# Kernel tuning notes

Hardware: AMD Instinct MI355X
Metric: run time of the kernel (lower is better)

The kernel has to match this reference:

```python
import jax, jax.numpy as jnp
import numpy as np

KERNEL_MUL = 2.0
KERNEL_NUM = 5


def setup_inputs() -> dict:
    key = jax.random.key(0)
    k1, k2 = jax.random.split(key)
    source = jax.random.normal(k1, (4096, 256), dtype=jnp.float32)
    target = jax.random.normal(k2, (4096, 256), dtype=jnp.float32)
    return {"source": source, "target": target}


def reference(source, target):
    n = source.shape[0]
    total = jnp.concatenate([source, target], axis=0)  # [2N, D]
    ns = total.shape[0]
    # Squared-L2 pairwise distances via the GEMM trick (avoids [2N,2N,D] blowup)
    sq = jnp.sum(total * total, axis=1)  # [2N]
    dist = sq[:, None] + sq[None, :] - 2.0 * (total @ total.T)  # [2N,2N]
    # bandwidth computed on detached distances (torch uses .data)
    bandwidth = jax.lax.stop_gradient(jnp.sum(dist)) / (ns * ns - ns)
    bandwidth = bandwidth / (KERNEL_MUL ** (KERNEL_NUM // 2))
    # multi-bandwidth Gaussian kernel sum (small fixed loop over KERNEL_NUM)
    kernels = jnp.zeros_like(dist)
    for i in range(KERNEL_NUM):
        kernels = kernels + jnp.exp(-dist / (bandwidth * (KERNEL_MUL ** i)))
    kernels = kernels / KERNEL_NUM
    XX = kernels[:n, :n]
    YY = kernels[n:, n:]
    XY = kernels[:n, n:]
    YX = kernels[n:, :n]
    # symmetric == 'yes' branch
    return jnp.mean(XX + YY - XY - YX) / 2.0
```

## Files before the change

### kernel.cpp

```cpp
#include <hip/hip_runtime.h>

#define NROWS 8192
#define NHALF 4096
#define DIM   256
#define NB_PREP 256
#define NTILES  64
#define NBLK    2080

typedef __attribute__((ext_vector_type(4))) float f32x4;

__device__ __forceinline__ const float* side_base(const float* src, const float* tgt, int row) {
    return (row < NHALF) ? (src + (size_t)row * DIM)
                         : (tgt + (size_t)(row - NHALF) * DIM);
}

__global__ __launch_bounds__(256) void prep_kernel(
        const float* __restrict__ src, const float* __restrict__ tgt,
        unsigned char* __restrict__ F8,
        float* __restrict__ sq, float* __restrict__ colpart, float* __restrict__ sqpart)
{
    int t = threadIdx.x;
    int lane = t & 63;
    int w = t >> 6;
    int wave = blockIdx.x * 4 + w;
    float cs0 = 0, cs1 = 0, cs2 = 0, cs3 = 0;
    double lss = 0.0;
    for (int r = wave; r < NROWS; r += NB_PREP * 4) {
        const float* p = side_base(src, tgt, r);
        float4 v = *(const float4*)(p + 4 * lane);
        cs0 += v.x; cs1 += v.y; cs2 += v.z; cs3 += v.w;
        int p01 = __builtin_amdgcn_cvt_pk_fp8_f32(v.x, v.y, 0, false);
        int pk  = __builtin_amdgcn_cvt_pk_fp8_f32(v.z, v.w, p01, true);
        *(unsigned*)(F8 + (size_t)r * DIM + 4 * lane) = (unsigned)pk;
        float d = v.x * v.x + v.y * v.y + v.z * v.z + v.w * v.w;
        #pragma unroll
        for (int off = 32; off > 0; off >>= 1) d += __shfl_xor(d, off);
        if (lane == 0) { sq[r] = d; lss += (double)d; }
    }
    __shared__ float csh[4][256];
    __shared__ double ssh[4];
    csh[w][4 * lane + 0] = cs0; csh[w][4 * lane + 1] = cs1;
    csh[w][4 * lane + 2] = cs2; csh[w][4 * lane + 3] = cs3;
    if (lane == 0) ssh[w] = lss;
    __syncthreads();
    colpart[blockIdx.x * 256 + t] = csh[0][t] + csh[1][t] + csh[2][t] + csh[3][t];
    if (t == 0) sqpart[blockIdx.x] = (float)(ssh[0] + ssh[1] + ssh[2] + ssh[3]);
}

__global__ void bw_kernel(const float* __restrict__ colpart,
                          const float* __restrict__ sqpart, float* __restrict__ qconst)
{
    __shared__ double red[256], red2[256];
    int t = threadIdx.x;
    double s = 0;
    for (int b = 0; b < NB_PREP; ++b) s += (double)colpart[b * 256 + t];
    red[t] = s * s;
    red2[t] = (double)sqpart[t];
    __syncthreads();
    for (int k = 128; k > 0; k >>= 1) {
        if (t < k) { red[t] += red[t + k]; red2[t] += red2[t + k]; }
        __syncthreads();
    }
    if (t == 0) {
        double ns = (double)NROWS;
        double sumdist = 2.0 * ns * red2[0] - 2.0 * red[0];
        double bw = sumdist / (ns * ns - ns) / 4.0;
        qconst[0] = (float)(1.4426950408889634 / (16.0 * bw));
    }
}

__device__ __forceinline__ int tri_cum(int b) {
    return b * NTILES - ((b * (b - 1)) >> 1);
}

__global__ __launch_bounds__(256) void mmd_main_kernel(
        const unsigned char* __restrict__ F8,
        const float* __restrict__ sq, const float* __restrict__ qc,
        float* __restrict__ partials)
{
    __shared__ alignas(16) char lds[65536];

    int wg = blockIdx.x;
    int rank = (wg & 7) * (NBLK / 8) + (wg >> 3);
    int by = (int)((129.0f - sqrtf(16641.0f - 8.0f * (float)rank)) * 0.5f);
    while (tri_cum(by + 1) <= rank) ++by;
    while (tri_cum(by) > rank) --by;
    int bx = by + (rank - tri_cum(by));

    int t = threadIdx.x;
    int rowBase = by * 128, colBase = bx * 128;
    int lane = t & 63, w = t >> 6;
    int wr = w >> 1, wc = w & 1;

    #pragma unroll
    for (int q = 0; q < 8; ++q) {
        int p = q * 4096 + t * 16;
        int row = p >> 8;
        int col = (p & 255) ^ ((row & 7) << 4);
        const char* ga = (const char*)F8 + (((size_t)(rowBase + row)) << 8) + col;
        const char* gb = (const char*)F8 + (((size_t)(colBase + row)) << 8) + col;
        __builtin_amdgcn_global_load_lds(
            (const __attribute__((address_space(1))) void*)ga,
            (__attribute__((address_space(3))) void*)(lds + p), 16, 0, 0);
        __builtin_amdgcn_global_load_lds(
            (const __attribute__((address_space(1))) void*)gb,
            (__attribute__((address_space(3))) void*)(lds + 32768 + p), 16, 0, 0);
    }
    __syncthreads();

    f32x4 acc[4][4];
    #pragma unroll
    for (int m = 0; m < 4; ++m)
        #pragma unroll
        for (int n = 0; n < 4; ++n) acc[m][n] = (f32x4)0.f;

    #pragma unroll
    for (int kk = 0; kk < 8; ++kk) {
        int kcol = kk * 32 + ((lane >> 4) << 3);
        long long af[4], bf[4];
        #pragma unroll
        for (int m = 0; m < 4; ++m) {
            int r = wr * 64 + m * 16 + (lane & 15);
            int off = ((r << 8) + kcol) ^ ((r & 7) << 4);
            af[m] = *(const long long*)(lds + off);
        }
        #pragma unroll
        for (int n = 0; n < 4; ++n) {
            int r = wc * 64 + n * 16 + (lane & 15);
            int off = ((r << 8) + kcol) ^ ((r & 7) << 4);
            bf[n] = *(const long long*)(lds + 32768 + off);
        }
        #pragma unroll
        for (int m = 0; m < 4; ++m)
            #pragma unroll
            for (int n = 0; n < 4; ++n)
                acc[m][n] = __builtin_amdgcn_mfma_f32_16x16x32_fp8_fp8(
                    af[m], bf[n], acc[m][n], 0, 0, 0);
    }

    float q = qc[0], twoq = 2.f * q;
    int rsub = (lane >> 4) * 4, csub = lane & 15;
    float nqa[4][4], qb[4];
    #pragma unroll
    for (int m = 0; m < 4; ++m)
        #pragma unroll
        for (int r = 0; r < 4; ++r)
            nqa[m][r] = -q * sq[rowBase + wr * 64 + m * 16 + rsub + r];
    #pragma unroll
    for (int n = 0; n < 4; ++n)
        qb[n] = q * sq[colBase + wc * 64 + n * 16 + csub];

    float psum = 0.f;
    #pragma unroll
    for (int m = 0; m < 4; ++m) {
        #pragma unroll
        for (int n = 0; n < 4; ++n) {
            #pragma unroll
            for (int r = 0; r < 4; ++r) {
                float arg = fmaf(acc[m][n][r], twoq, nqa[m][r] - qb[n]);
                float e4 = __builtin_amdgcn_exp2f(arg);
                float e3 = e4 * e4, e2 = e3 * e3, e1 = e2 * e2, e0 = e1 * e1;
                psum += ((e4 + e3) + (e2 + e1)) + e0;
            }
        }
    }

    #pragma unroll
    for (int off = 32; off > 0; off >>= 1) psum += __shfl_xor(psum, off);
    __syncthreads();
    float* redw = (float*)lds;
    if (lane == 0) redw[w] = psum;
    __syncthreads();
    if (t == 0) {
        float sign = ((rowBase < NHALF) == (colBase < NHALF)) ? 1.f : -1.f;
        float wgt = (bx == by) ? 1.f : 2.f;
        partials[rank] = sign * wgt * (redw[0] + redw[1] + redw[2] + redw[3]);
    }
}

__global__ void finalize_kernel(const float* __restrict__ partials, int n,
                                float* __restrict__ out)
{
    __shared__ double red[256];
    int t = threadIdx.x;
    double s = 0;
    for (int i = t; i < n; i += 256) s += (double)partials[i];
    red[t] = s;
    __syncthreads();
    for (int k = 128; k > 0; k >>= 1) { if (t < k) red[t] += red[t + k]; __syncthreads(); }
    if (t == 0) {
        double nn = (double)NHALF;
        out[0] = (float)(red[0] / 5.0 / (2.0 * nn * nn));
    }
}

extern "C" void kernel_launch(void* const* d_in, const int* in_sizes, int n_in,
                              void* d_out, int out_size, void* d_ws, size_t ws_size,
                              hipStream_t stream) {
    const float* src = (const float*)d_in[0];
    const float* tgt = (const float*)d_in[1];
    float* out = (float*)d_out;
    char* ws = (char*)d_ws;

    float*         colpart  = (float*)(ws + 0);
    float*         sqpart   = (float*)(ws + 262144);
    float*         qconst   = (float*)(ws + 263168);
    float*         sq       = (float*)(ws + 264192);
    float*         partials = (float*)(ws + 297984);
    unsigned char* F8       = (unsigned char*)(ws + 524288);

    prep_kernel<<<NB_PREP, 256, 0, stream>>>(src, tgt, F8, sq, colpart, sqpart);
    bw_kernel<<<1, 256, 0, stream>>>(colpart, sqpart, qconst);
    mmd_main_kernel<<<NBLK, 256, 0, stream>>>(F8, sq, qconst, partials);
    finalize_kernel<<<1, 256, 0, stream>>>(partials, NBLK, out);
}
```

Before: 51.13 us.

## Use K=128 scaled FP8 MFMA and stage K in two halves with smaller LDS

The main GEMM now uses the 16x16x128 f8f6f4 scaled MFMA with unit scales, replacing four 16x16x32 FP8 MFMAs per output tile, and loads 32-byte fragments with two 16-byte LDS reads. K is staged in two 128-byte chunks, which halves the LDS footprint to 32KB, and launch bounds now request 4 workgroups per CU to raise occupancy. The cost is an extra barrier and load phase between chunks with no overlap, plus some register pressure from the wider fragments.

```diff
diff --git a/kernel.cpp b/kernel.cpp
--- a/kernel.cpp
+++ b/kernel.cpp
@@ -8,6 +8,8 @@
 #define NBLK    2080
 
 typedef __attribute__((ext_vector_type(4))) float f32x4;
+typedef __attribute__((ext_vector_type(4))) int   v4i;
+typedef __attribute__((ext_vector_type(8))) int   v8i;
 
 __device__ __forceinline__ const float* side_base(const float* src, const float* tgt, int row) {
     return (row < NHALF) ? (src + (size_t)row * DIM)
@@ -73,12 +75,36 @@
     return b * NTILES - ((b * (b - 1)) >> 1);
 }
 
-__global__ __launch_bounds__(256) void mmd_main_kernel(
+__device__ __forceinline__ v8i load_frag(const char* base, int r, int kbase) {
+    int sw = (r & 7) << 4;
+    v4i lo = *(const v4i*)(base + (r << 7) + (kbase ^ sw));
+    v4i hi = *(const v4i*)(base + (r << 7) + ((kbase + 16) ^ sw));
+    v8i out;
+    out[0] = lo[0]; out[1] = lo[1]; out[2] = lo[2]; out[3] = lo[3];
+    out[4] = hi[0]; out[5] = hi[1]; out[6] = hi[2]; out[7] = hi[3];
+    return out;
+}
+
+__device__ __forceinline__ f32x4 mfma_k128(v8i a, v8i b, f32x4 c) {
+#if __has_builtin(__builtin_amdgcn_mfma_scale_f32_16x16x128_f8f6f4)
+    return __builtin_amdgcn_mfma_scale_f32_16x16x128_f8f6f4(
+        a, b, c, 0, 0, 0, 0x7F7F7F7F, 0, 0x7F7F7F7F);
+#else
+    const long long* av = (const long long*)&a;
+    const long long* bv = (const long long*)&b;
+    #pragma unroll
+    for (int i = 0; i < 4; ++i)
+        c = __builtin_amdgcn_mfma_f32_16x16x32_fp8_fp8(av[i], bv[i], c, 0, 0, 0);
+    return c;
+#endif
+}
+
+__global__ __launch_bounds__(256, 4) void mmd_main_kernel(
         const unsigned char* __restrict__ F8,
         const float* __restrict__ sq, const float* __restrict__ qc,
         float* __restrict__ partials)
 {
-    __shared__ alignas(16) char lds[65536];
+    __shared__ alignas(16) char lds[32768];
 
     int wg = blockIdx.x;
     int rank = (wg & 7) * (NBLK / 8) + (wg >> 3);
@@ -91,22 +117,7 @@
     int rowBase = by * 128, colBase = bx * 128;
     int lane = t & 63, w = t >> 6;
     int wr = w >> 1, wc = w & 1;
-
-    #pragma unroll
-    for (int q = 0; q < 8; ++q) {
-        int p = q * 4096 + t * 16;
-        int row = p >> 8;
-        int col = (p & 255) ^ ((row & 7) << 4);
-        const char* ga = (const char*)F8 + (((size_t)(rowBase + row)) << 8) + col;
-        const char* gb = (const char*)F8 + (((size_t)(colBase + row)) << 8) + col;
-        __builtin_amdgcn_global_load_lds(
-            (const __attribute__((address_space(1))) void*)ga,
-            (__attribute__((address_space(3))) void*)(lds + p), 16, 0, 0);
-        __builtin_amdgcn_global_load_lds(
-            (const __attribute__((address_space(1))) void*)gb,
-            (__attribute__((address_space(3))) void*)(lds + 32768 + p), 16, 0, 0);
-    }
-    __syncthreads();
+    int kbase = (lane >> 4) << 5;
 
     f32x4 acc[4][4];
     #pragma unroll
@@ -115,27 +126,35 @@
         for (int n = 0; n < 4; ++n) acc[m][n] = (f32x4)0.f;
 
     #pragma unroll
-    for (int kk = 0; kk < 8; ++kk) {
-        int kcol = kk * 32 + ((lane >> 4) << 3);
-        long long af[4], bf[4];
+    for (int kc = 0; kc < 2; ++kc) {
+        if (kc) __syncthreads();
+        #pragma unroll
+        for (int q = 0; q < 4; ++q) {
+            int p = q * 4096 + t * 16;
+            int row = p >> 7;
+            int col = (p & 127) ^ ((row & 7) << 4);
+            const char* ga = (const char*)F8 + (((size_t)(rowBase + row)) << 8) + kc * 128 + col;
+            const char* gb = (const char*)F8 + (((size_t)(colBase + row)) << 8) + kc * 128 + col;
+            __builtin_amdgcn_global_load_lds(
+                (const __attribute__((address_space(1))) void*)ga,
+                (__attribute__((address_space(3))) void*)(lds + p), 16, 0, 0);
+            __builtin_amdgcn_global_load_lds(
+                (const __attribute__((address_space(1))) void*)gb,
+                (__attribute__((address_space(3))) void*)(lds + 16384 + p), 16, 0, 0);
+        }
+        __syncthreads();
+
+        v8i bf[4];
+        #pragma unroll
+        for (int n = 0; n < 4; ++n)
+            bf[n] = load_frag(lds + 16384, wc * 64 + n * 16 + (lane & 15), kbase);
         #pragma unroll
         for (int m = 0; m < 4; ++m) {
-            int r = wr * 64 + m * 16 + (lane & 15);
-            int off = ((r << 8) + kcol) ^ ((r & 7) << 4);
-            af[m] = *(const long long*)(lds + off);
-        }
-        #pragma unroll
-        for (int n = 0; n < 4; ++n) {
-            int r = wc * 64 + n * 16 + (lane & 15);
-            int off = ((r << 8) + kcol) ^ ((r & 7) << 4);
-            bf[n] = *(const long long*)(lds + 32768 + off);
-        }
-        #pragma unroll
-        for (int m = 0; m < 4; ++m)
+            v8i af = load_frag(lds, wr * 64 + m * 16 + (lane & 15), kbase);
             #pragma unroll
             for (int n = 0; n < 4; ++n)
-                acc[m][n] = __builtin_amdgcn_mfma_f32_16x16x32_fp8_fp8(
-                    af[m], bf[n], acc[m][n], 0, 0, 0);
+                acc[m][n] = mfma_k128(af, bf[n], acc[m][n]);
+        }
     }
 
     float q = qc[0], twoq = 2.f * q;
```

After: 46.86 us. -8.4%, faster.
